# Optimization experiments

Hardware: AMD Instinct MI355X
Metric: run time of the kernel (lower is better)

The kernel has to match this reference:

```python
import jax, jax.numpy as jnp
import numpy as np

B, L, H, E = 8, 1024, 8, 64
S, D = 1024, 64


def fp(x):
    # power-norm with p=2: norm(x) * x^2 / norm(x^2)
    norm = jnp.sqrt(jnp.sum(x * x, axis=-1, keepdims=True))
    px = x * x  # x^p, p=2
    pnorm = jnp.sqrt(jnp.sum(px * px, axis=-1, keepdims=True))
    return norm * px / pnorm


def phi_p(x):
    return fp(jax.nn.relu(x))


def setup_inputs() -> dict:
    key = jax.random.key(0)
    kq, kk, kv = jax.random.split(key, 3)
    queries = jax.random.normal(kq, (B, L, H, E), dtype=jnp.float32)
    keys = jax.random.normal(kk, (B, S, H, E), dtype=jnp.float32)
    values = jax.random.normal(kv, (B, S, H, D), dtype=jnp.float32)
    # all-False mask: masked_fill(-inf) + fp() would NaN otherwise (see notes)
    attn_mask = jnp.zeros((B, 1, L, S), dtype=bool)
    return {"queries": queries, "keys": keys, "values": values, "attn_mask": attn_mask}


def reference(queries, keys, values, attn_mask):
    qt = phi_p(queries)              # [B,L,H,E]
    kt = phi_p(keys)                 # [B,S,H,E]
    scores = jnp.einsum('blhe,bshe->bhls', qt, kt)  # [B,H,L,S]
    scores = jnp.where(attn_mask, -jnp.inf, scores)  # mask_flag=True path
    # NB: original computes scale = 1/sqrt(E) but never applies it.
    A = jax.nn.softmax(fp(scores), axis=-1)  # dropout is identity at eval
    V = jnp.einsum('bhls,bshd->blhd', A, values)  # [B,L,H,D]
    return V
```

## Files before the change

### kernel.cpp

```cpp
#include <hip/hip_runtime.h>
#include <hip/hip_bf16.h>


#define B_ 8
#define L_ 1024
#define H_ 8
#define E_ 64
#define S_ 1024
#define D_ 64
#define BH_ 64

typedef _Float16 f16_t;
typedef _Float16 f16x8 __attribute__((ext_vector_type(8)));
typedef _Float16 f16x4v __attribute__((ext_vector_type(4)));
typedef float f32x4 __attribute__((ext_vector_type(4)));

#define MFMA16F(a, b, c) __builtin_amdgcn_mfma_f32_16x16x32_f16(a, b, c, 0, 0, 0)
#define GLDS16(g, l)                                                        \
  __builtin_amdgcn_global_load_lds(                                         \
      (const __attribute__((address_space(1))) void*)(g),                   \
      (__attribute__((address_space(3))) void*)(l), 16, 0, 0)

#if __has_builtin(__builtin_amdgcn_exp2f)
#define EXP2(x) __builtin_amdgcn_exp2f(x)
#else
#define EXP2(x) exp2f(x)
#endif

__global__ __launch_bounds__(256) void prep_kernel(
    const float* __restrict__ q, const float* __restrict__ k,
    const float* __restrict__ v, f16_t* __restrict__ qf,
    f16_t* __restrict__ kf, f16_t* __restrict__ vt) {
  __shared__ float tile[32][68];
  int bid = blockIdx.x;
  if (bid < 8192) {
    int row = bid * 16 + (threadIdx.x >> 4);
    int p = threadIdx.x & 15;
    const float* src;
    f16_t* dst;
    int r = row;
    if (r < B_ * L_ * H_) { src = q; dst = qf; }
    else { r -= B_ * L_ * H_; src = k; dst = kf; }
    int b = r >> 13;
    int l = (r >> 3) & 1023;
    int h = r & 7;
    float4 x = ((const float4*)(src + (size_t)r * 64))[p];
    float s0 = fmaxf(x.x, 0.f) * fmaxf(x.x, 0.f);
    float s1 = fmaxf(x.y, 0.f) * fmaxf(x.y, 0.f);
    float s2 = fmaxf(x.z, 0.f) * fmaxf(x.z, 0.f);
    float s3 = fmaxf(x.w, 0.f) * fmaxf(x.w, 0.f);
    float sum2 = (s0 + s1) + (s2 + s3);
    float sum4 = fmaf(s0, s0, s1 * s1) + fmaf(s2, s2, s3 * s3);
#pragma unroll
    for (int off = 1; off < 16; off <<= 1) {
      sum2 += __shfl_xor(sum2, off, 64);
      sum4 += __shfl_xor(sum4, off, 64);
    }
    float sc = (sum4 > 0.f) ? sqrtf(sum2 / sum4) : 0.f;
    f16x4v o = {(f16_t)(sc * s0), (f16_t)(sc * s1), (f16_t)(sc * s2),
                (f16_t)(sc * s3)};
    int c = p >> 1, e = (p & 1) * 4;
    int col = (((c ^ (l & 7)) << 3) | e);
    *(f16x4v*)(dst + ((size_t)(b * H_ + h) * 1024 + l) * 64 + col) = o;
  } else {
    int vb = bid - 8192;
    int bh = vb >> 5;
    int st = vb & 31;
    int b = bh >> 3, h = bh & 7;
    int t = threadIdx.x;
    int sl = t >> 3, dp = t & 7;
    const float* src =
        v + (((size_t)(b * S_ + st * 32 + sl) * H_ + h) * D_) + dp * 8;
    float4 f0 = ((const float4*)src)[0];
    float4 f1 = ((const float4*)src)[1];
    *(float4*)&tile[sl][dp * 8] = f0;
    *(float4*)&tile[sl][dp * 8 + 4] = f1;
    __syncthreads();
    int d = t >> 2, sc = t & 3;
    f16_t tmp[8];
#pragma unroll
    for (int j = 0; j < 8; ++j) tmp[j] = (f16_t)tile[sc * 8 + j][d];
    f16_t* dst = vt + (((size_t)bh * 32 + st) * 64 + d) * 32 + sc * 8;
    *(uint4*)dst = *(const uint4*)tmp;
  }
}

__global__ __launch_bounds__(256, 4) void attn_kernel(
    const f16_t* __restrict__ qf, const f16_t* __restrict__ kf,
    const f16_t* __restrict__ vt, float* __restrict__ out) {
  __shared__ __align__(16) f16_t k_t[2][2048];
  __shared__ __align__(16) f16_t v_t[2][2048];
  __shared__ __align__(16) f16_t wbuf[4][16 * 40];

  int bh = blockIdx.x & 63;
  int qb = blockIdx.x >> 6;
  int b = bh >> 3, h = bh & 7;
  int tid = threadIdx.x;
  int wave = tid >> 6, lane = tid & 63;
  int g = lane >> 4, n = lane & 15;

  const f16_t* qf_b = qf + ((size_t)bh * L_ + qb * 64) * 64;
  const f16_t* kf_b = kf + (size_t)bh * S_ * 64;
  const f16_t* vt_b = vt + (size_t)bh * 32 * 2048;

  int arow = wave * 16 + n;
  int qoff = arow * 64 + ((g ^ (n & 7)) << 3);
  f16x8 qa0 = *(const f16x8*)(qf_b + qoff);
  f16x8 qa1 = *(const f16x8*)(qf_b + (qoff ^ 32));

  int koff = n * 64 + ((g ^ (n & 7)) << 3);
  int lds_o = tid * 8;

  const f32x4 fzero = {0.f, 0.f, 0.f, 0.f};
  f32x4 acc2 = fzero, acc4 = fzero, mx = fzero;

  const f16_t* kg = kf_b;
#pragma unroll 2
  for (int t = 0; t < 32; ++t) {
    f16x8 b00 = *(const f16x8*)(kg + koff);
    f16x8 b01 = *(const f16x8*)(kg + (koff ^ 32));
    f16x8 b10 = *(const f16x8*)(kg + koff + 1024);
    f16x8 b11 = *(const f16x8*)(kg + (koff ^ 32) + 1024);
    kg += 2048;
    f32x4 sc0 = MFMA16F(qa0, b00, fzero);
    sc0 = MFMA16F(qa1, b01, sc0);
    f32x4 sc1 = MFMA16F(qa0, b10, fzero);
    sc1 = MFMA16F(qa1, b11, sc1);
    f32x4 t0 = sc0 * sc0, t1 = sc1 * sc1;
    acc2 += t0 + t1;
    acc4 += t0 * t0;
    acc4 += t1 * t1;
    mx = __builtin_elementwise_max(mx, __builtin_elementwise_max(t0, t1));
  }
  float a2[4], a4[4], m2[4];
#pragma unroll
  for (int r = 0; r < 4; ++r) { a2[r] = acc2[r]; a4[r] = acc4[r]; m2[r] = mx[r]; }
#pragma unroll
  for (int off = 1; off < 16; off <<= 1)
#pragma unroll
    for (int r = 0; r < 4; ++r) {
      a2[r] += __shfl_xor(a2[r], off, 64);
      a4[r] += __shfl_xor(a4[r], off, 64);
      m2[r] = fmaxf(m2[r], __shfl_xor(m2[r], off, 64));
    }
  const float LOG2E = 1.44269504f;
  f32x4 c2v, cm2v;
#pragma unroll
  for (int r = 0; r < 4; ++r) {
    float cr = (a4[r] > 0.f) ? (sqrtf(a2[r] / a4[r]) * LOG2E) : 0.f;
    c2v[r] = cr;
    cm2v[r] = cr * m2[r];
  }

  f32x4 pv[4];
#pragma unroll
  for (int dg = 0; dg < 4; ++dg) pv[dg] = fzero;
  f32x4 denv = fzero;
  f16_t* wb = wbuf[wave];

  GLDS16(kf_b + lds_o, &k_t[0][lds_o]);
  GLDS16(vt_b + lds_o, &v_t[0][lds_o]);
  for (int t = 0; t < 32; ++t) {
    __syncthreads();
    if (t < 31) {
      int go = (t + 1) * 2048 + lds_o;
      int bs = (t + 1) & 1;
      GLDS16(kf_b + go, &k_t[bs][lds_o]);
      GLDS16(vt_b + go, &v_t[bs][lds_o]);
    }
    const f16_t* kt = k_t[t & 1];
    const f16_t* vl = v_t[t & 1];
    f16x8 vb[4];
#pragma unroll
    for (int dg = 0; dg < 4; ++dg)
      vb[dg] = *(const f16x8*)(vl + n * 32 + dg * 512 + g * 8);
    f16x8 b00 = *(const f16x8*)(kt + koff);
    f16x8 b01 = *(const f16x8*)(kt + (koff ^ 32));
    f16x8 b10 = *(const f16x8*)(kt + koff + 1024);
    f16x8 b11 = *(const f16x8*)(kt + (koff ^ 32) + 1024);
    f32x4 sc0 = MFMA16F(qa0, b00, fzero);
    sc0 = MFMA16F(qa1, b01, sc0);
    f32x4 sc1 = MFMA16F(qa0, b10, fzero);
    sc1 = MFMA16F(qa1, b11, sc1);
    f32x4 e0 = sc0 * sc0 * c2v - cm2v;
    f32x4 e1 = sc1 * sc1 * c2v - cm2v;
    f32x4 w0, w1;
#pragma unroll
    for (int r = 0; r < 4; ++r) { w0[r] = EXP2(e0[r]); w1[r] = EXP2(e1[r]); }
    denv += w0 + w1;
#pragma unroll
    for (int r = 0; r < 4; ++r) {
      wb[(g * 4 + r) * 40 + n] = (f16_t)w0[r];
      wb[(g * 4 + r) * 40 + 16 + n] = (f16_t)w1[r];
    }
    f16x8 wa = *(const f16x8*)(wb + n * 40 + g * 8);
#pragma unroll
    for (int dg = 0; dg < 4; ++dg) pv[dg] = MFMA16F(wa, vb[dg], pv[dg]);
  }
  float den[4];
#pragma unroll
  for (int r = 0; r < 4; ++r) den[r] = denv[r];
#pragma unroll
  for (int off = 1; off < 16; off <<= 1)
#pragma unroll
    for (int r = 0; r < 4; ++r) den[r] += __shfl_xor(den[r], off, 64);
#pragma unroll
  for (int r = 0; r < 4; ++r) {
    float inv = 1.f / den[r];
    int l = qb * 64 + wave * 16 + g * 4 + r;
    float* op = out + (((size_t)b * L_ + l) * H_ + h) * D_;
#pragma unroll
    for (int dg = 0; dg < 4; ++dg) op[dg * 16 + n] = pv[dg][r] * inv;
  }
}

extern "C" void kernel_launch(void* const* d_in, const int* in_sizes, int n_in,
                              void* d_out, int out_size, void* d_ws, size_t ws_size,
                              hipStream_t stream) {
  const float* q = (const float*)d_in[0];
  const float* k = (const float*)d_in[1];
  const float* v = (const float*)d_in[2];
  float* out = (float*)d_out;

  const size_t NE = (size_t)B_ * L_ * H_ * E_;
  f16_t* qf = (f16_t*)d_ws;
  f16_t* kf = qf + NE;
  f16_t* vt = kf + NE;

  prep_kernel<<<8192 + 2048, 256, 0, stream>>>(q, k, v, qf, kf, vt);
  attn_kernel<<<BH_ * (L_ / 64), 256, 0, stream>>>(qf, kf, vt, out);
}
```

Before: 161.9 us.

## Give each wave a private LDS K/V buffer and drop block barriers

Each wave now loads the whole K/V tile into its own private LDS region, replacing the block-wide __syncthreads with per-wave vmcnt/lgkmcnt waits. The tile is read into registers before the next tile's async load overwrites the same single buffer, so the load overlaps the exp/MFMA work. This removes cross-wave barrier stalls. In exchange it issues four times the global-to-LDS traffic per block and quadruples LDS use for K/V, which can lower occupancy.

```diff
diff --git a/kernel.cpp b/kernel.cpp
--- a/kernel.cpp
+++ b/kernel.cpp
@@ -20,6 +20,8 @@
   __builtin_amdgcn_global_load_lds(                                         \
       (const __attribute__((address_space(1))) void*)(g),                   \
       (__attribute__((address_space(3))) void*)(l), 16, 0, 0)
+#define WAIT_VM0() __asm__ __volatile__("s_waitcnt vmcnt(0)" ::: "memory")
+#define WAIT_LGKM0() __asm__ __volatile__("s_waitcnt lgkmcnt(0)" ::: "memory")
 
 #if __has_builtin(__builtin_amdgcn_exp2f)
 #define EXP2(x) __builtin_amdgcn_exp2f(x)
@@ -88,8 +90,8 @@
 __global__ __launch_bounds__(256, 4) void attn_kernel(
     const f16_t* __restrict__ qf, const f16_t* __restrict__ kf,
     const f16_t* __restrict__ vt, float* __restrict__ out) {
-  __shared__ __align__(16) f16_t k_t[2][2048];
-  __shared__ __align__(16) f16_t v_t[2][2048];
+  __shared__ __align__(16) f16_t kbuf[4][2048];
+  __shared__ __align__(16) f16_t vbuf[4][2048];
   __shared__ __align__(16) f16_t wbuf[4][16 * 40];
 
   int bh = blockIdx.x & 63;
@@ -98,6 +100,7 @@
   int tid = threadIdx.x;
   int wave = tid >> 6, lane = tid & 63;
   int g = lane >> 4, n = lane & 15;
+  int lane8 = lane * 8;
 
   const f16_t* qf_b = qf + ((size_t)bh * L_ + qb * 64) * 64;
   const f16_t* kf_b = kf + (size_t)bh * S_ * 64;
@@ -109,19 +112,19 @@
   f16x8 qa1 = *(const f16x8*)(qf_b + (qoff ^ 32));
 
   int koff = n * 64 + ((g ^ (n & 7)) << 3);
-  int lds_o = tid * 8;
+  int voff = n * 32 + g * 8;
 
   const f32x4 fzero = {0.f, 0.f, 0.f, 0.f};
   f32x4 acc2 = fzero, acc4 = fzero, mx = fzero;
 
-  const f16_t* kg = kf_b;
+  const f16_t* kg1 = kf_b;
 #pragma unroll 2
   for (int t = 0; t < 32; ++t) {
-    f16x8 b00 = *(const f16x8*)(kg + koff);
-    f16x8 b01 = *(const f16x8*)(kg + (koff ^ 32));
-    f16x8 b10 = *(const f16x8*)(kg + koff + 1024);
-    f16x8 b11 = *(const f16x8*)(kg + (koff ^ 32) + 1024);
-    kg += 2048;
+    f16x8 b00 = *(const f16x8*)(kg1 + koff);
+    f16x8 b01 = *(const f16x8*)(kg1 + (koff ^ 32));
+    f16x8 b10 = *(const f16x8*)(kg1 + koff + 1024);
+    f16x8 b11 = *(const f16x8*)(kg1 + (koff ^ 32) + 1024);
+    kg1 += 2048;
     f32x4 sc0 = MFMA16F(qa0, b00, fzero);
     sc0 = MFMA16F(qa1, b01, sc0);
     f32x4 sc1 = MFMA16F(qa0, b10, fzero);
@@ -157,31 +160,38 @@
   for (int dg = 0; dg < 4; ++dg) pv[dg] = fzero;
   f32x4 denv = fzero;
   f16_t* wb = wbuf[wave];
-
-  GLDS16(kf_b + lds_o, &k_t[0][lds_o]);
-  GLDS16(vt_b + lds_o, &v_t[0][lds_o]);
+  f16_t* kb_l = kbuf[wave];
+  f16_t* vb_l = vbuf[wave];
+
+#pragma unroll
+  for (int i = 0; i < 4; ++i) {
+    GLDS16(kf_b + i * 512 + lane8, kb_l + i * 512 + lane8);
+    GLDS16(vt_b + i * 512 + lane8, vb_l + i * 512 + lane8);
+  }
   for (int t = 0; t < 32; ++t) {
-    __syncthreads();
+    WAIT_VM0();
+    f16x8 kb0 = *(const f16x8*)(kb_l + koff);
+    f16x8 kb1 = *(const f16x8*)(kb_l + (koff ^ 32));
+    f16x8 kb2 = *(const f16x8*)(kb_l + koff + 1024);
+    f16x8 kb3 = *(const f16x8*)(kb_l + (koff ^ 32) + 1024);
+    f16x8 vb[4];
+#pragma unroll
+    for (int dg = 0; dg < 4; ++dg)
+      vb[dg] = *(const f16x8*)(vb_l + voff + dg * 512);
+    WAIT_LGKM0();
     if (t < 31) {
-      int go = (t + 1) * 2048 + lds_o;
-      int bs = (t + 1) & 1;
-      GLDS16(kf_b + go, &k_t[bs][lds_o]);
-      GLDS16(vt_b + go, &v_t[bs][lds_o]);
-    }
-    const f16_t* kt = k_t[t & 1];
-    const f16_t* vl = v_t[t & 1];
-    f16x8 vb[4];
-#pragma unroll
-    for (int dg = 0; dg < 4; ++dg)
-      vb[dg] = *(const f16x8*)(vl + n * 32 + dg * 512 + g * 8);
-    f16x8 b00 = *(const f16x8*)(kt + koff);
-    f16x8 b01 = *(const f16x8*)(kt + (koff ^ 32));
-    f16x8 b10 = *(const f16x8*)(kt + koff + 1024);
-    f16x8 b11 = *(const f16x8*)(kt + (koff ^ 32) + 1024);
-    f32x4 sc0 = MFMA16F(qa0, b00, fzero);
-    sc0 = MFMA16F(qa1, b01, sc0);
-    f32x4 sc1 = MFMA16F(qa0, b10, fzero);
-    sc1 = MFMA16F(qa1, b11, sc1);
+      const f16_t* kg = kf_b + (t + 1) * 2048;
+      const f16_t* vg = vt_b + (t + 1) * 2048;
+#pragma unroll
+      for (int i = 0; i < 4; ++i) {
+        GLDS16(kg + i * 512 + lane8, kb_l + i * 512 + lane8);
+        GLDS16(vg + i * 512 + lane8, vb_l + i * 512 + lane8);
+      }
+    }
+    f32x4 sc0 = MFMA16F(qa0, kb0, fzero);
+    sc0 = MFMA16F(qa1, kb1, sc0);
+    f32x4 sc1 = MFMA16F(qa0, kb2, fzero);
+    sc1 = MFMA16F(qa1, kb3, sc1);
     f32x4 e0 = sc0 * sc0 * c2v - cm2v;
     f32x4 e1 = sc1 * sc1 * c2v - cm2v;
     f32x4 w0, w1;
```

Measured after the change: 176.3 us. 1.09x slower.
